# Kernel optimization log

Measured on AMD Instinct MI355X. Metric: run time of the kernel, lower is better.

The kernel has to match this reference:

```python
import jax, jax.numpy as jnp
import numpy as np


def _conv(x, w, pad):
    # NCHW conv, stride 1, symmetric padding
    return jax.lax.conv_general_dilated(
        x, w, window_strides=(1, 1), padding=[(pad, pad), (pad, pad)],
        dimension_numbers=("NCHW", "OIHW", "NCHW"))


def setup_inputs() -> dict:
    key = jax.random.key(0)
    ks = jax.random.split(key, 8)
    B, L_I, L_H, L_Q, IM, N_ACT = 64, 2, 150, 10, 128, 5
    return {
        "input_view": jax.random.normal(ks[0], (B, L_I, IM, IM), jnp.float32),
        "state_x": jax.random.randint(ks[1], (B,), 0, IM),
        "state_y": jax.random.randint(ks[2], (B,), 0, IM),
        "k": 50,
        "h_w": jax.random.normal(ks[3], (L_H, L_I, 3, 3), jnp.float32) * 0.05,
        "h_b": jnp.zeros((L_H,), jnp.float32),
        "r_w": jax.random.normal(ks[4], (1, L_H, 1, 1), jnp.float32) * 0.05,
        "q_w": jax.random.normal(ks[5], (L_Q, 1, 3, 3), jnp.float32) * 0.1,
        "w": jax.random.normal(ks[6], (L_Q, 1, 3, 3), jnp.float32) * 0.1,
        "fc_w": jax.random.normal(ks[7], (N_ACT, L_Q), jnp.float32) * 0.1,
    }


def reference(input_view, state_x, state_y, k, h_w, h_b, r_w, q_w, w, fc_w):
    # process_input: h -> r -> q -> v
    h = _conv(input_view, h_w, 1) + h_b[None, :, None, None]   # (B, l_h, H, W)
    r = _conv(h, r_w, 0)                                        # (B, 1,  H, W)
    q = _conv(r, q_w, 1)                                        # (B, l_q, H, W)
    v = jnp.max(q, axis=1, keepdims=True)                       # (B, 1,  H, W)

    # value_iteration: k-1 updates of v, then final q
    wq = jnp.concatenate([q_w, w], axis=1)                      # (l_q, 2, 3, 3)

    def body(v, _):
        qi = _conv(jnp.concatenate([r, v], axis=1), wq, 1)
        return jnp.max(qi, axis=1, keepdims=True), None

    v, _ = jax.lax.scan(body, v, None, length=k - 1)
    q = _conv(jnp.concatenate([r, v], axis=1), wq, 1)           # (B, l_q, H, W)

    # get_action: gather q at agent states, project to action logits
    B = q.shape[0]
    q_out = q[jnp.arange(B), :, state_x, state_y]               # (B, l_q)
    logits = q_out @ fc_w.T                                     # (B, 5)
    return logits
```

## Files before the change

kernel.cpp:

```cpp
#include <hip/hip_runtime.h>


#define IM 128
#define Bn 64
#define LQ 10
#define LH 150
#define NACT 5
#define TW 136
#define NTHR 1024

#define RV 19
#define NRQ 35
#define NR 37

__global__ __launch_bounds__(NTHR) void prep_r(
    const float* __restrict__ in, const float* __restrict__ h_w,
    const float* __restrict__ h_b, const float* __restrict__ r_w,
    const float* __restrict__ q_w, float* __restrict__ rglob,
    float* __restrict__ v0g) {
    __shared__ float in_t[2][36][IM];
    __shared__ float r_loc[34][TW];
    __shared__ float wbuf[19];

    const int bid = blockIdx.x;
    const int b   = bid >> 2;
    const int y0  = (bid & 3) * 32;
    const int tid = threadIdx.x;
    const float* inb = in + ((size_t)b * 2 << 14);

    if (tid < 18) {
        float s = 0.f;
        for (int c = 0; c < LH; ++c) s = fmaf(r_w[c], h_w[c * 18 + tid], s);
        wbuf[tid] = s;
    } else if (tid == 18) {
        float s = 0.f;
        for (int c = 0; c < LH; ++c) s = fmaf(r_w[c], h_b[c], s);
        wbuf[18] = s;
    }

    for (int i = tid; i < 2 * 36 * 32; i += NTHR) {
        int ch = i / (36 * 32);
        int rest = i - ch * (36 * 32);
        int ir = rest >> 5, x4 = (rest & 31) * 4;
        int yi = y0 - 2 + ir;
        float4 v = make_float4(0.f, 0.f, 0.f, 0.f);
        if (yi >= 0 && yi < IM) v = *(const float4*)&inb[(ch << 14) + (yi << 7) + x4];
        *(float4*)&in_t[ch][ir][x4] = v;
    }
    __syncthreads();

    for (int i = tid; i < 34 * IM; i += NTHR) {
        int rr = i >> 7, x = i & 127;
        int yr = y0 - 1 + rr;
        float acc = 0.f;
        if (yr >= 0 && yr < IM) {
            acc = wbuf[18];
#pragma unroll
            for (int ch = 0; ch < 2; ++ch)
#pragma unroll
                for (int dy = 0; dy < 3; ++dy) {
                    const float* row = &in_t[ch][rr + dy][0];
                    float l = (x > 0) ? row[x - 1] : 0.f;
                    float m = row[x];
                    float r2 = (x < IM - 1) ? row[x + 1] : 0.f;
                    acc = fmaf(wbuf[ch * 9 + dy * 3 + 0], l,
                          fmaf(wbuf[ch * 9 + dy * 3 + 1], m,
                          fmaf(wbuf[ch * 9 + dy * 3 + 2], r2, acc)));
                }
        }
        r_loc[rr][x + 4] = acc;
    }
    if (tid < 34) { r_loc[tid][3] = 0.f; r_loc[tid][132] = 0.f; }
    __syncthreads();

    float* rg = rglob + ((size_t)b << 14);
    for (int i = tid; i < 32 * IM; i += NTHR) {
        int rr = 1 + (i >> 7), x = i & 127;
        rg[((y0 + (i >> 7)) << 7) + x] = r_loc[rr][x + 4];
    }
    float* vg = v0g + ((size_t)b << 14);
    for (int i = tid; i < 32 * IM; i += NTHR) {
        int vr = i >> 7, x = i & 127;
        float nv = -3.4e38f;
#pragma unroll
        for (int a = 0; a < LQ; ++a) {
            float acc = 0.f;
#pragma unroll
            for (int dy = 0; dy < 3; ++dy)
#pragma unroll
                for (int dx = 0; dx < 3; ++dx)
                    acc = fmaf(q_w[a * 9 + dy * 3 + dx], r_loc[vr + dy][x + 3 + dx], acc);
            nv = fmaxf(nv, acc);
        }
        vg[((y0 + vr) << 7) + x] = nv;
    }
}

template<int WR>
__device__ __forceinline__ float act9(const float* __restrict__ wt, float rqv,
                                      const float (&win)[WR][3], int i) {
    float acc = rqv;
    acc = fmaf(wt[0], win[i][0],     acc);
    acc = fmaf(wt[1], win[i][1],     acc);
    acc = fmaf(wt[2], win[i][2],     acc);
    acc = fmaf(wt[3], win[i + 1][0], acc);
    acc = fmaf(wt[4], win[i + 1][1], acc);
    acc = fmaf(wt[5], win[i + 1][2], acc);
    acc = fmaf(wt[6], win[i + 2][0], acc);
    acc = fmaf(wt[7], win[i + 2][1], acc);
    acc = fmaf(wt[8], win[i + 2][2], acc);
    return acc;
}

template<int OWN, int SR>
__global__ __launch_bounds__(NTHR) void vin_band(
    const float* __restrict__ rglob, const float* __restrict__ q_w,
    const float* __restrict__ w, const float* __restrict__ vin_g,
    float* __restrict__ vout_g, const int* __restrict__ sx)
{
    constexpr int DATA = OWN + 16;
    constexpr int ROWS = 8 * SR + 3;
    static_assert(8 * SR >= DATA - 1, "strips must cover all required rows");
    __shared__ float v_t[2][ROWS][TW];
    __shared__ float r_t[ROWS][TW];

    const int bid  = blockIdx.x;
    const int b    = bid >> 2;
    const int tid  = threadIdx.x;
    const int c    = tid & 127;
    const int k    = tid >> 7;
    const int base_k = 1 + SR * k;

    const int Y = sx[b];
    int base = Y - 2 * OWN;
    if (base < 0) base = 0;
    if (base > IM - 4 * OWN) base = IM - 4 * OWN;
    const int o = base + OWN * (bid & 3);

    const float* rg = rglob + ((size_t)b << 14);
    for (int i = tid; i < (DATA + 2) * 32; i += NTHR) {
        int rr = i >> 5, x4 = (i & 31) * 4;
        int yr = o - 9 + rr;
        float4 v = make_float4(0.f, 0.f, 0.f, 0.f);
        if (yr >= 0 && yr < IM) v = *(const float4*)&rg[(yr << 7) + x4];
        *(float4*)&r_t[rr][x4 + 4] = v;
    }
    if (tid < ROWS) { r_t[tid][3] = 0.f; r_t[tid][132] = 0.f; }

    const float* vb = vin_g + ((size_t)b << 14);
    for (int i = tid; i < DATA * 32; i += NTHR) {
        int tr = 1 + (i >> 5), x4 = (i & 31) * 4;
        int yv = o + tr - 9;
        float4 v = make_float4(0.f, 0.f, 0.f, 0.f);
        if (yv >= 0 && yv < IM) v = *(const float4*)&vb[(yv << 7) + x4];
        *(float4*)&v_t[0][tr][x4 + 4] = v;
    }
    if (tid < TW) { v_t[0][0][tid] = 0.f; v_t[1][0][tid] = 0.f; }
    if (tid < ROWS) {
        v_t[0][tid][3] = 0.f; v_t[0][tid][132] = 0.f;
        v_t[1][tid][3] = 0.f; v_t[1][tid][132] = 0.f;
    }
    __syncthreads();

    float rq[SR][LQ];
    {
        float win[SR + 2][3];
#pragma unroll
        for (int r = 0; r < SR + 2; ++r) {
            win[r][0] = r_t[base_k - 1 + r][c + 3];
            win[r][1] = r_t[base_k - 1 + r][c + 4];
            win[r][2] = r_t[base_k - 1 + r][c + 5];
        }
#pragma unroll
        for (int a = 0; a < LQ; ++a)
#pragma unroll
            for (int i = 0; i < SR; ++i)
                rq[i][a] = act9<SR + 2>(q_w + a * 9, 0.f, win, i);
    }

#pragma unroll 1
    for (int t = 1; t <= 8; ++t) {
        const int p = (t - 1) & 1;
        const float (*vin)[TW] = v_t[p];
        float (*vout)[TW] = v_t[p ^ 1];
        const int lo = 1 + t, hi = DATA - t;
        __syncthreads();
        float win[SR + 2][3];
#pragma unroll
        for (int r = 0; r < SR + 2; ++r) {
            win[r][0] = vin[base_k - 1 + r][c + 3];
            win[r][1] = vin[base_k - 1 + r][c + 4];
            win[r][2] = vin[base_k - 1 + r][c + 5];
        }
#pragma unroll
        for (int i = 0; i < SR; ++i) {
            const int tr = base_k + i;
            if (tr >= lo && tr <= hi) {
                float a0 = act9<SR + 2>(w + 0 * 9, rq[i][0], win, i);
                float a1 = act9<SR + 2>(w + 1 * 9, rq[i][1], win, i);
                float a2 = act9<SR + 2>(w + 2 * 9, rq[i][2], win, i);
                float g0 = fmaxf(fmaxf(a0, a1), a2);
                float a3 = act9<SR + 2>(w + 3 * 9, rq[i][3], win, i);
                float a4 = act9<SR + 2>(w + 4 * 9, rq[i][4], win, i);
                float a5 = act9<SR + 2>(w + 5 * 9, rq[i][5], win, i);
                float g1 = fmaxf(fmaxf(a3, a4), a5);
                float a6 = act9<SR + 2>(w + 6 * 9, rq[i][6], win, i);
                float a7 = act9<SR + 2>(w + 7 * 9, rq[i][7], win, i);
                float a8 = act9<SR + 2>(w + 8 * 9, rq[i][8], win, i);
                float g2 = fmaxf(fmaxf(a6, a7), a8);
                float a9 = act9<SR + 2>(w + 9 * 9, rq[i][9], win, i);
                float nv = fmaxf(fmaxf(fmaxf(g0, g1), g2), a9);
                int yv = o + tr - 9;
                vout[tr][c + 4] = (yv >= 0 && yv < IM) ? nv : 0.f;
            }
        }
    }
    __syncthreads();

    float* vo = vout_g + ((size_t)b << 14);
#pragma unroll
    for (int i = 0; i < SR; ++i) {
        int tr = base_k + i;
        if (tr >= 9 && tr <= OWN + 8) {
            int yv = o + tr - 9;
            vo[(yv << 7) + c] = v_t[0][tr][c + 4];
        }
    }
}

__global__ __launch_bounds__(NTHR) void cone_finish(
    const float* __restrict__ rglob, const float* __restrict__ q_w,
    const float* __restrict__ w, const float* __restrict__ v32g,
    const int* __restrict__ sx, const int* __restrict__ sy,
    const float* __restrict__ fc_w, float* __restrict__ out)
{
    __shared__ float v_c[2][2 * RV + 1][2 * RV + 2];
    __shared__ float rq_c[NRQ][NRQ][11];
    __shared__ float r_c[NR][NR + 3];

    const int b   = blockIdx.x;
    const int tid = threadIdx.x;
    const int Y   = sx[b];
    const int X   = sy[b];

    const float* rg = rglob + ((size_t)b << 14);
    for (int p = tid; p < NR * NR; p += NTHR) {
        int i = p / NR, j = p - i * NR;
        int iy = Y - 18 + i, ix = X - 18 + j;
        r_c[i][j] = (iy >= 0 && iy < IM && ix >= 0 && ix < IM) ? rg[(iy << 7) + ix] : 0.f;
    }
    const float* vg = v32g + ((size_t)b << 14);
    for (int p = tid; p < (2 * RV + 1) * (2 * RV + 1); p += NTHR) {
        int i = p / (2 * RV + 1), j = p - i * (2 * RV + 1);
        int iy = Y - RV + i, ix = X - RV + j;
        v_c[0][i][j] = (iy >= 0 && iy < IM && ix >= 0 && ix < IM) ? vg[(iy << 7) + ix] : 0.f;
    }
    __syncthreads();

    for (int p = tid; p < NRQ * NRQ; p += NTHR) {
        int i2 = p / NRQ, j2 = p - i2 * NRQ;
#pragma unroll
        for (int a = 0; a < LQ; ++a) {
            const float* qt = q_w + a * 9;
            float acc = 0.f;
#pragma unroll
            for (int dy = 0; dy < 3; ++dy)
#pragma unroll
                for (int dx = 0; dx < 3; ++dx)
                    acc = fmaf(qt[dy * 3 + dx], r_c[i2 + dy][j2 + dx], acc);
            rq_c[i2][j2][a] = acc;
        }
    }

    int par = 0;
    const int rr0 = tid >> 6, cc = tid & 63;
#pragma unroll 1
    for (int t = 33; t <= 49; ++t) {
        const int rho = 50 - t;
        const int W   = 2 * rho + 1;
        const int off = RV - rho;
        __syncthreads();
        const float (*vp)[2 * RV + 2] = v_c[par];
        float (*vo)[2 * RV + 2] = v_c[par ^ 1];
        for (int rr = rr0; rr < W; rr += 16) {
            if (cc < W) {
                int lr = off + rr, lc = off + cc;
                float v00 = vp[lr - 1][lc - 1], v01 = vp[lr - 1][lc], v02 = vp[lr - 1][lc + 1];
                float v10 = vp[lr    ][lc - 1], v11 = vp[lr    ][lc], v12 = vp[lr    ][lc + 1];
                float v20 = vp[lr + 1][lc - 1], v21 = vp[lr + 1][lc], v22 = vp[lr + 1][lc + 1];
                const float* rqp = &rq_c[lr - 2][lc - 2][0];
                float nv = -3.4e38f;
#pragma unroll
                for (int a = 0; a < LQ; ++a) {
                    const float* wt = w + a * 9;
                    float acc = rqp[a];
                    acc = fmaf(wt[0], v00, acc); acc = fmaf(wt[1], v01, acc);
                    acc = fmaf(wt[2], v02, acc); acc = fmaf(wt[3], v10, acc);
                    acc = fmaf(wt[4], v11, acc); acc = fmaf(wt[5], v12, acc);
                    acc = fmaf(wt[6], v20, acc); acc = fmaf(wt[7], v21, acc);
                    acc = fmaf(wt[8], v22, acc);
                    nv = fmaxf(nv, acc);
                }
                int iy = Y - RV + lr, ix = X - RV + lc;
                vo[lr][lc] = (iy >= 0 && iy < IM && ix >= 0 && ix < IM) ? nv : 0.f;
            }
        }
        par ^= 1;
    }
    __syncthreads();

    if (tid < NACT) {
        const float (*vf)[2 * RV + 2] = v_c[par];
        float s = 0.f;
#pragma unroll
        for (int a = 0; a < LQ; ++a) {
            const float* wt = w + a * 9;
            float acc = rq_c[RV - 2][RV - 2][a];
#pragma unroll
            for (int dy = 0; dy < 3; ++dy)
#pragma unroll
                for (int dx = 0; dx < 3; ++dx)
                    acc = fmaf(wt[dy * 3 + dx], vf[RV - 1 + dy][RV - 1 + dx], acc);
            s = fmaf(acc, fc_w[tid * LQ + a], s);
        }
        out[b * NACT + tid] = s;
    }
}

extern "C" void kernel_launch(void* const* d_in, const int* in_sizes, int n_in,
                              void* d_out, int out_size, void* d_ws, size_t ws_size,
                              hipStream_t stream) {
    const float* input = (const float*)d_in[0];
    const int*   sx    = (const int*)d_in[1];
    const int*   sy    = (const int*)d_in[2];
    const float* h_w   = (const float*)d_in[4];
    const float* h_b   = (const float*)d_in[5];
    const float* r_w   = (const float*)d_in[6];
    const float* q_w   = (const float*)d_in[7];
    const float* w     = (const float*)d_in[8];
    const float* fc_w  = (const float*)d_in[9];
    float* out = (float*)d_out;

    char* ws = (char*)d_ws;
    float* vgA   = (float*)ws;
    float* vgB   = (float*)(ws + (4u << 20));
    float* rglob = (float*)(ws + (8u << 20));

    prep_r<<<Bn * 4, NTHR, 0, stream>>>(input, h_w, h_b, r_w, q_w, rglob, vgA);

    vin_band<22, 5><<<Bn * 4, NTHR, 0, stream>>>(rglob, q_w, w, vgA, vgB, sx);
    vin_band<18, 5><<<Bn * 4, NTHR, 0, stream>>>(rglob, q_w, w, vgB, vgA, sx);
    vin_band<14, 4><<<Bn * 4, NTHR, 0, stream>>>(rglob, q_w, w, vgA, vgB, sx);
    vin_band<10, 4><<<Bn * 4, NTHR, 0, stream>>>(rglob, q_w, w, vgB, vgA, sx);

    cone_finish<<<Bn, NTHR, 0, stream>>>(rglob, q_w, w, vgA, sx, sy, fc_w, out);
}
```

Baseline: 153.1 us.

## Fuse r/v0 preparation into first value-iteration band kernel

Removes the separate prep_r kernel. The first vin_band instantiation now computes the collapsed h→r convolution for its own band rows directly from the input, and derives the initial v from the q activations it already holds in registers. This drops one kernel launch and the global write and read of v0. It also restricts r computation to the rows the agent-centred bands actually need. An input tile is unioned with the v buffers in shared memory, and halo rows of r are written redundantly by neighbouring blocks.

Result: faster. 146.9 us (-4.1%).

```diff
diff --git a/kernel.cpp b/kernel.cpp
--- a/kernel.cpp
+++ b/kernel.cpp
@@ -12,89 +12,6 @@
 #define RV 19
 #define NRQ 35
 #define NR 37
-
-__global__ __launch_bounds__(NTHR) void prep_r(
-    const float* __restrict__ in, const float* __restrict__ h_w,
-    const float* __restrict__ h_b, const float* __restrict__ r_w,
-    const float* __restrict__ q_w, float* __restrict__ rglob,
-    float* __restrict__ v0g) {
-    __shared__ float in_t[2][36][IM];
-    __shared__ float r_loc[34][TW];
-    __shared__ float wbuf[19];
-
-    const int bid = blockIdx.x;
-    const int b   = bid >> 2;
-    const int y0  = (bid & 3) * 32;
-    const int tid = threadIdx.x;
-    const float* inb = in + ((size_t)b * 2 << 14);
-
-    if (tid < 18) {
-        float s = 0.f;
-        for (int c = 0; c < LH; ++c) s = fmaf(r_w[c], h_w[c * 18 + tid], s);
-        wbuf[tid] = s;
-    } else if (tid == 18) {
-        float s = 0.f;
-        for (int c = 0; c < LH; ++c) s = fmaf(r_w[c], h_b[c], s);
-        wbuf[18] = s;
-    }
-
-    for (int i = tid; i < 2 * 36 * 32; i += NTHR) {
-        int ch = i / (36 * 32);
-        int rest = i - ch * (36 * 32);
-        int ir = rest >> 5, x4 = (rest & 31) * 4;
-        int yi = y0 - 2 + ir;
-        float4 v = make_float4(0.f, 0.f, 0.f, 0.f);
-        if (yi >= 0 && yi < IM) v = *(const float4*)&inb[(ch << 14) + (yi << 7) + x4];
-        *(float4*)&in_t[ch][ir][x4] = v;
-    }
-    __syncthreads();
-
-    for (int i = tid; i < 34 * IM; i += NTHR) {
-        int rr = i >> 7, x = i & 127;
-        int yr = y0 - 1 + rr;
-        float acc = 0.f;
-        if (yr >= 0 && yr < IM) {
-            acc = wbuf[18];
-#pragma unroll
-            for (int ch = 0; ch < 2; ++ch)
-#pragma unroll
-                for (int dy = 0; dy < 3; ++dy) {
-                    const float* row = &in_t[ch][rr + dy][0];
-                    float l = (x > 0) ? row[x - 1] : 0.f;
-                    float m = row[x];
-                    float r2 = (x < IM - 1) ? row[x + 1] : 0.f;
-                    acc = fmaf(wbuf[ch * 9 + dy * 3 + 0], l,
-                          fmaf(wbuf[ch * 9 + dy * 3 + 1], m,
-                          fmaf(wbuf[ch * 9 + dy * 3 + 2], r2, acc)));
-                }
-        }
-        r_loc[rr][x + 4] = acc;
-    }
-    if (tid < 34) { r_loc[tid][3] = 0.f; r_loc[tid][132] = 0.f; }
-    __syncthreads();
-
-    float* rg = rglob + ((size_t)b << 14);
-    for (int i = tid; i < 32 * IM; i += NTHR) {
-        int rr = 1 + (i >> 7), x = i & 127;
-        rg[((y0 + (i >> 7)) << 7) + x] = r_loc[rr][x + 4];
-    }
-    float* vg = v0g + ((size_t)b << 14);
-    for (int i = tid; i < 32 * IM; i += NTHR) {
-        int vr = i >> 7, x = i & 127;
-        float nv = -3.4e38f;
-#pragma unroll
-        for (int a = 0; a < LQ; ++a) {
-            float acc = 0.f;
-#pragma unroll
-            for (int dy = 0; dy < 3; ++dy)
-#pragma unroll
-                for (int dx = 0; dx < 3; ++dx)
-                    acc = fmaf(q_w[a * 9 + dy * 3 + dx], r_loc[vr + dy][x + 3 + dx], acc);
-            nv = fmaxf(nv, acc);
-        }
-        vg[((y0 + vr) << 7) + x] = nv;
-    }
-}
 
 template<int WR>
 __device__ __forceinline__ float act9(const float* __restrict__ wt, float rqv,
@@ -112,17 +29,23 @@
     return acc;
 }
 
-template<int OWN, int SR>
+template<int OWN, int SR, bool FIRST>
 __global__ __launch_bounds__(NTHR) void vin_band(
-    const float* __restrict__ rglob, const float* __restrict__ q_w,
+    const float* __restrict__ in, const float* __restrict__ h_w,
+    const float* __restrict__ h_b, const float* __restrict__ r_w,
+    float* __restrict__ rglob, const float* __restrict__ q_w,
     const float* __restrict__ w, const float* __restrict__ vin_g,
     float* __restrict__ vout_g, const int* __restrict__ sx)
 {
     constexpr int DATA = OWN + 16;
     constexpr int ROWS = 8 * SR + 3;
     static_assert(8 * SR >= DATA - 1, "strips must cover all required rows");
-    __shared__ float v_t[2][ROWS][TW];
+    __shared__ union {
+        float in_t[2][DATA + 4][IM];
+        float v_t[2][ROWS][TW];
+    } U;
     __shared__ float r_t[ROWS][TW];
+    __shared__ float wbuf[19];
 
     const int bid  = blockIdx.x;
     const int b    = bid >> 2;
@@ -137,30 +60,76 @@
     if (base > IM - 4 * OWN) base = IM - 4 * OWN;
     const int o = base + OWN * (bid & 3);
 
-    const float* rg = rglob + ((size_t)b << 14);
-    for (int i = tid; i < (DATA + 2) * 32; i += NTHR) {
-        int rr = i >> 5, x4 = (i & 31) * 4;
-        int yr = o - 9 + rr;
-        float4 v = make_float4(0.f, 0.f, 0.f, 0.f);
-        if (yr >= 0 && yr < IM) v = *(const float4*)&rg[(yr << 7) + x4];
-        *(float4*)&r_t[rr][x4 + 4] = v;
-    }
-    if (tid < ROWS) { r_t[tid][3] = 0.f; r_t[tid][132] = 0.f; }
-
-    const float* vb = vin_g + ((size_t)b << 14);
-    for (int i = tid; i < DATA * 32; i += NTHR) {
-        int tr = 1 + (i >> 5), x4 = (i & 31) * 4;
-        int yv = o + tr - 9;
-        float4 v = make_float4(0.f, 0.f, 0.f, 0.f);
-        if (yv >= 0 && yv < IM) v = *(const float4*)&vb[(yv << 7) + x4];
-        *(float4*)&v_t[0][tr][x4 + 4] = v;
-    }
-    if (tid < TW) { v_t[0][0][tid] = 0.f; v_t[1][0][tid] = 0.f; }
-    if (tid < ROWS) {
-        v_t[0][tid][3] = 0.f; v_t[0][tid][132] = 0.f;
-        v_t[1][tid][3] = 0.f; v_t[1][tid][132] = 0.f;
-    }
-    __syncthreads();
+    if (FIRST) {
+        if (tid < 18) {
+            float s = 0.f;
+            for (int cc2 = 0; cc2 < LH; ++cc2) s = fmaf(r_w[cc2], h_w[cc2 * 18 + tid], s);
+            wbuf[tid] = s;
+        } else if (tid == 18) {
+            float s = 0.f;
+            for (int cc2 = 0; cc2 < LH; ++cc2) s = fmaf(r_w[cc2], h_b[cc2], s);
+            wbuf[18] = s;
+        }
+        const float* inb = in + ((size_t)b * 2 << 14);
+        for (int i = tid; i < 2 * (DATA + 4) * 32; i += NTHR) {
+            int ch = i / ((DATA + 4) * 32);
+            int rest = i - ch * ((DATA + 4) * 32);
+            int ir = rest >> 5, x4 = (rest & 31) * 4;
+            int yi = o - 10 + ir;
+            float4 v = make_float4(0.f, 0.f, 0.f, 0.f);
+            if (yi >= 0 && yi < IM) v = *(const float4*)&inb[(ch << 14) + (yi << 7) + x4];
+            *(float4*)&U.in_t[ch][ir][x4] = v;
+        }
+        __syncthreads();
+        for (int i = tid; i < (DATA + 2) * IM; i += NTHR) {
+            int rr = i >> 7, x = i & 127;
+            int yr = o - 9 + rr;
+            float acc = 0.f;
+            if (yr >= 0 && yr < IM) {
+                acc = wbuf[18];
+#pragma unroll
+                for (int ch = 0; ch < 2; ++ch)
+#pragma unroll
+                    for (int dy = 0; dy < 3; ++dy) {
+                        const float* row = &U.in_t[ch][rr + dy][0];
+                        float l = (x > 0) ? row[x - 1] : 0.f;
+                        float m = row[x];
+                        float r2 = (x < IM - 1) ? row[x + 1] : 0.f;
+                        acc = fmaf(wbuf[ch * 9 + dy * 3 + 0], l,
+                              fmaf(wbuf[ch * 9 + dy * 3 + 1], m,
+                              fmaf(wbuf[ch * 9 + dy * 3 + 2], r2, acc)));
+                    }
+            }
+            r_t[rr][x + 4] = acc;
+        }
+        if (tid < ROWS) { r_t[tid][3] = 0.f; r_t[tid][132] = 0.f; }
+        __syncthreads();
+        float* rg = rglob + ((size_t)b << 14);
+        for (int i = tid; i < (DATA + 2) * IM; i += NTHR) {
+            int rr = i >> 7, x = i & 127;
+            int yr = o - 9 + rr;
+            if (yr >= 0 && yr < IM) rg[(yr << 7) + x] = r_t[rr][x + 4];
+        }
+    } else {
+        const float* rg = rglob + ((size_t)b << 14);
+        for (int i = tid; i < (DATA + 2) * 32; i += NTHR) {
+            int rr = i >> 5, x4 = (i & 31) * 4;
+            int yr = o - 9 + rr;
+            float4 v = make_float4(0.f, 0.f, 0.f, 0.f);
+            if (yr >= 0 && yr < IM) v = *(const float4*)&rg[(yr << 7) + x4];
+            *(float4*)&r_t[rr][x4 + 4] = v;
+        }
+        if (tid < ROWS) { r_t[tid][3] = 0.f; r_t[tid][132] = 0.f; }
+        const float* vb = vin_g + ((size_t)b << 14);
+        for (int i = tid; i < DATA * 32; i += NTHR) {
+            int tr = 1 + (i >> 5), x4 = (i & 31) * 4;
+            int yv = o + tr - 9;
+            float4 v = make_float4(0.f, 0.f, 0.f, 0.f);
+            if (yv >= 0 && yv < IM) v = *(const float4*)&vb[(yv << 7) + x4];
+            *(float4*)&U.v_t[0][tr][x4 + 4] = v;
+        }
+        __syncthreads();
+    }
 
     float rq[SR][LQ];
     {
@@ -178,11 +147,29 @@
                 rq[i][a] = act9<SR + 2>(q_w + a * 9, 0.f, win, i);
     }
 
+    if (FIRST) {
+#pragma unroll
+        for (int i = 0; i < SR; ++i) {
+            int tr = base_k + i;
+            int yv = o + tr - 9;
+            float g0 = fmaxf(fmaxf(rq[i][0], rq[i][1]), rq[i][2]);
+            float g1 = fmaxf(fmaxf(rq[i][3], rq[i][4]), rq[i][5]);
+            float g2 = fmaxf(fmaxf(rq[i][6], rq[i][7]), rq[i][8]);
+            float nv = fmaxf(fmaxf(fmaxf(g0, g1), g2), rq[i][9]);
+            U.v_t[0][tr][c + 4] = (yv >= 0 && yv < IM) ? nv : 0.f;
+        }
+    }
+    if (tid < TW) { U.v_t[0][0][tid] = 0.f; U.v_t[1][0][tid] = 0.f; }
+    if (tid < ROWS) {
+        U.v_t[0][tid][3] = 0.f; U.v_t[0][tid][132] = 0.f;
+        U.v_t[1][tid][3] = 0.f; U.v_t[1][tid][132] = 0.f;
+    }
+
 #pragma unroll 1
     for (int t = 1; t <= 8; ++t) {
         const int p = (t - 1) & 1;
-        const float (*vin)[TW] = v_t[p];
-        float (*vout)[TW] = v_t[p ^ 1];
+        const float (*vin)[TW] = U.v_t[p];
+        float (*vout)[TW] = U.v_t[p ^ 1];
         const int lo = 1 + t, hi = DATA - t;
         __syncthreads();
         float win[SR + 2][3];
@@ -223,7 +210,7 @@
         int tr = base_k + i;
         if (tr >= 9 && tr <= OWN + 8) {
             int yv = o + tr - 9;
-            vo[(yv << 7) + c] = v_t[0][tr][c + 4];
+            vo[(yv << 7) + c] = U.v_t[0][tr][c + 4];
         }
     }
 }
@@ -346,12 +333,14 @@
     float* vgB   = (float*)(ws + (4u << 20));
     float* rglob = (float*)(ws + (8u << 20));
 
-    prep_r<<<Bn * 4, NTHR, 0, stream>>>(input, h_w, h_b, r_w, q_w, rglob, vgA);
-
-    vin_band<22, 5><<<Bn * 4, NTHR, 0, stream>>>(rglob, q_w, w, vgA, vgB, sx);
-    vin_band<18, 5><<<Bn * 4, NTHR, 0, stream>>>(rglob, q_w, w, vgB, vgA, sx);
-    vin_band<14, 4><<<Bn * 4, NTHR, 0, stream>>>(rglob, q_w, w, vgA, vgB, sx);
-    vin_band<10, 4><<<Bn * 4, NTHR, 0, stream>>>(rglob, q_w, w, vgB, vgA, sx);
+    vin_band<22, 5, true ><<<Bn * 4, NTHR, 0, stream>>>(input, h_w, h_b, r_w, rglob,
+                                                        q_w, w, nullptr, vgB, sx);
+    vin_band<18, 5, false><<<Bn * 4, NTHR, 0, stream>>>(input, h_w, h_b, r_w, rglob,
+                                                        q_w, w, vgB, vgA, sx);
+    vin_band<14, 4, false><<<Bn * 4, NTHR, 0, stream>>>(input, h_w, h_b, r_w, rglob,
+                                                        q_w, w, vgA, vgB, sx);
+    vin_band<10, 4, false><<<Bn * 4, NTHR, 0, stream>>>(input, h_w, h_b, r_w, rglob,
+                                                        q_w, w, vgB, vgA, sx);
 
     cone_finish<<<Bn, NTHR, 0, stream>>>(rglob, q_w, w, vgA, sx, sy, fc_w, out);
 }
```
